# Performance work log

Measured on AMD Instinct MI355X. Metric: run time of the kernel, lower is better.

The kernel has to match this reference:

```python
import jax, jax.numpy as jnp
import numpy as np

B, N, C, H = 1, 4096, 512, 8
S = 64  # sqrt(N), static


def setup_inputs() -> dict:
    key = jax.random.key(0)
    ks = jax.random.split(key, 4)
    d = C // H
    return {
        "x": jax.random.normal(ks[0], (B, N, C), dtype=jnp.float32),
        "num_heads": H,
        "bias": jnp.zeros((1,), dtype=jnp.float32),  # unused in original forward
        "scale": jnp.asarray(d ** -0.5, dtype=jnp.float32),
        "Wqkv": jax.random.normal(ks[1], (3 * C, C), dtype=jnp.float32) * (C ** -0.5),
        "bqkv": jnp.zeros((3 * C,), dtype=jnp.float32),
        "Wproj": jax.random.normal(ks[2], (C, C), dtype=jnp.float32) * (C ** -0.5),
        "bproj": jnp.zeros((C,), dtype=jnp.float32),
    }


def reference(x, num_heads, bias, scale, Wqkv, bqkv, Wproj, bproj):
    b, n, c = x.shape
    d = c // num_heads
    # fused QKV projection: [b, n, 3c] -> [3, b, h, n, d]
    qkv = (x @ Wqkv.T + bqkv).reshape(b, n, 3, num_heads, d).transpose(2, 0, 3, 1, 4)
    q, k, v = qkv[0] * scale, qkv[1], qkv[2]
    attn = jax.nn.softmax(jnp.einsum("bhnd,bhmd->bhnm", q, k), axis=-1)
    out = jnp.einsum("bhnm,bhmd->bhnd", attn, v)
    out = out.transpose(0, 2, 1, 3).reshape(b, n, c)
    out = out @ Wproj.T + bproj
    return out.reshape(b, S, S, c)
```

## Files before the change

### kernel.cpp

```cpp
#include <hip/hip_runtime.h>
#include <stdint.h>

#define NTOK 4096
#define CDIM 512
#define HEADS 8
#define DHEAD 64
#define PHEAD (NTOK * DHEAD)

typedef __bf16 bf16x8 __attribute__((ext_vector_type(8)));
typedef float f32x4 __attribute__((ext_vector_type(4)));

__device__ __forceinline__ unsigned short bfbits(float f) {
    return __builtin_bit_cast(unsigned short, (__bf16)f);
}

__device__ __forceinline__ f32x4 mfma32(bf16x8 a, bf16x8 b, f32x4 c) {
    return __builtin_amdgcn_mfma_f32_16x16x32_bf16(a, b, c, 0, 0, 0);
}

__device__ __forceinline__ void stage8(unsigned short* dst, const float* src) {
    const float4 v0 = *(const float4*)src;
    const float4 v1 = *(const float4*)(src + 4);
    ushort4 o0, o1;
    o0.x = bfbits(v0.x); o0.y = bfbits(v0.y); o0.z = bfbits(v0.z); o0.w = bfbits(v0.w);
    o1.x = bfbits(v1.x); o1.y = bfbits(v1.y); o1.z = bfbits(v1.z); o1.w = bfbits(v1.w);
    *(ushort4*)dst = o0;
    *(ushort4*)(dst + 4) = o1;
}

__global__ __launch_bounds__(256) void gemm_qkv(
    const float* __restrict__ A,
    const float* __restrict__ Bm,
    const float* __restrict__ bias,
    const float* __restrict__ scale_p,
    unsigned short* __restrict__ qkv_out)
{
    __shared__ __align__(16) unsigned short smem[64 * 136];
    unsigned short* lA = smem;
    unsigned short* lB = smem + 2048;

    const int tid = threadIdx.x;
    const int mBase = blockIdx.y * 64, nBase = blockIdx.x * 128;
    const int lane = tid & 63;
    const int w = __builtin_amdgcn_readfirstlane(tid >> 6);
    const int l16 = lane & 15, quad = lane >> 4;
    const int srow = tid >> 2, scol = (tid & 3) * 8;

    f32x4 acc[4][2] = {};

    for (int kt = 0; kt < CDIM; kt += 32) {
        __syncthreads();
        stage8(&lA[srow * 32 + scol], &A[(size_t)(mBase + srow) * CDIM + kt + scol]);
#pragma unroll
        for (int p = 0; p < 2; ++p) {
            const int r = p * 64 + srow;
            stage8(&lB[r * 32 + scol], &Bm[(size_t)(nBase + r) * CDIM + kt + scol]);
        }
        __syncthreads();

        bf16x8 af[4], bfr[2];
#pragma unroll
        for (int i = 0; i < 4; ++i)
            af[i] = *(const bf16x8*)&lA[(i * 16 + l16) * 32 + quad * 8];
#pragma unroll
        for (int j = 0; j < 2; ++j)
            bfr[j] = *(const bf16x8*)&lB[(w * 32 + j * 16 + l16) * 32 + quad * 8];
#pragma unroll
        for (int i = 0; i < 4; ++i)
#pragma unroll
            for (int j = 0; j < 2; ++j)
                acc[i][j] = mfma32(af[i], bfr[j], acc[i][j]);
    }

    const int three = nBase >> 9;
    const float scl = scale_p[0] * 1.44269504f;
    const float mul = (three == 0) ? scl : 1.0f;

    __syncthreads();
#pragma unroll
    for (int i = 0; i < 4; ++i)
#pragma unroll
        for (int j = 0; j < 2; ++j)
#pragma unroll
            for (int r = 0; r < 4; ++r) {
                const int rl = i * 16 + quad * 4 + r;
                const int cl = w * 32 + j * 16 + l16;
                const float v = (acc[i][j][r] + bias[nBase + cl]) * mul;
                smem[rl * 136 + cl] = bfbits(v);
            }
    __syncthreads();

    const size_t base3 = (size_t)three * (PHEAD * HEADS);
    if (three < 2) {
#pragma unroll
        for (int pass = 0; pass < 4; ++pass) {
            const int idx = pass * 256 + tid;
            const int rl16 = idx & 15, qc = (idx >> 4) & 7;
            const int hsel = (idx >> 7) & 1, t16l = (idx >> 8) & 3;
            const uint4 d = *(const uint4*)&smem[(t16l * 16 + rl16) * 136 + hsel * 64 + qc * 8];
            const int hh = ((nBase >> 6) + hsel) & 7;
            const int t16 = (mBase >> 4) + t16l;
            const size_t dst = base3 + (size_t)hh * PHEAD +
                (size_t)(((t16 * 2 + (qc >> 2)) * 64 + (qc & 3) * 16 + rl16) * 8);
            *(uint4*)&qkv_out[dst] = d;
        }
    } else {
#pragma unroll
        for (int pass = 0; pass < 4; ++pass) {
            const int idx = pass * 256 + tid;
            const int l16t = idx & 15, quadt = (idx >> 4) & 3;
            const int dt = (idx >> 6) & 3, k32l = (idx >> 8) & 1, hsel = (idx >> 9) & 1;
            const int col = hsel * 64 + dt * 16 + l16t;
            unsigned short o8[8];
#pragma unroll
            for (int e = 0; e < 4; ++e) {
                o8[e]     = smem[(k32l * 32 + quadt * 4 + e) * 136 + col];
                o8[e + 4] = smem[(k32l * 32 + 16 + quadt * 4 + e) * 136 + col];
            }
            const int hh = ((nBase >> 6) + hsel) & 7;
            const int k32 = (mBase >> 5) + k32l;
            const size_t dst = base3 + (size_t)hh * PHEAD +
                (size_t)(((k32 * 4 + dt) * 64 + quadt * 16 + l16t) * 8);
            *(uint4*)&qkv_out[dst] = *(uint4*)o8;
        }
    }
}

__global__ __launch_bounds__(256, 4) void flash6_k(
    const unsigned short* __restrict__ qf,
    const unsigned short* __restrict__ kf,
    const unsigned short* __restrict__ vf,
    unsigned short* __restrict__ attn_out)
{
    __shared__ float ldsO[4][32][68];
    __shared__ float sml[4][32];

    const int tid = threadIdx.x;
    const int lane = tid & 63;
    const int w = __builtin_amdgcn_readfirstlane(tid >> 6);
    const int l16 = lane & 15, quad = lane >> 4;
    const int h = blockIdx.x, qb = blockIdx.y;

    const unsigned short* qh = qf + (size_t)h * PHEAD;
    const unsigned short* kb = kf + (size_t)h * PHEAD + w * 65536;
    const unsigned short* vb = vf + (size_t)h * PHEAD + w * 65536;

    bf16x8 qfr[2][2];
#pragma unroll
    for (int qt = 0; qt < 2; ++qt)
#pragma unroll
        for (int d2 = 0; d2 < 2; ++d2)
            qfr[qt][d2] = *(const bf16x8*)&qh[((qb * 2 + qt) * 2 + d2) * 512 + lane * 8];

    bf16x8 ones;
#pragma unroll
    for (int j = 0; j < 8; ++j) ones[j] = (__bf16)1.0f;

    f32x4 oacc[4][2] = {};
    f32x4 lacc[2] = {};

    bf16x8 kA[4], kB[4];
#pragma unroll
    for (int i = 0; i < 4; ++i)
        kA[i] = *(const bf16x8*)&kb[i * 512 + lane * 8];

    auto body = [&](int g, bf16x8* kuse, bf16x8* kload) {
#pragma unroll
        for (int i = 0; i < 4; ++i)
            kload[i] = *(const bf16x8*)&kb[(g + 1) * 2048 + i * 512 + lane * 8];
        bf16x8 vc[4];
#pragma unroll
        for (int i = 0; i < 4; ++i)
            vc[i] = *(const bf16x8*)&vb[g * 2048 + i * 512 + lane * 8];

        f32x4 s[2][2];
#pragma unroll
        for (int kt = 0; kt < 2; ++kt)
#pragma unroll
            for (int qt = 0; qt < 2; ++qt) {
                f32x4 a = {};
                a = mfma32(kuse[kt * 2 + 0], qfr[qt][0], a);
                a = mfma32(kuse[kt * 2 + 1], qfr[qt][1], a);
                s[kt][qt] = a;
            }

        bf16x8 pf[2];
#pragma unroll
        for (int qt = 0; qt < 2; ++qt) {
            bf16x8 pb;
#pragma unroll
            for (int kt = 0; kt < 2; ++kt)
#pragma unroll
                for (int r = 0; r < 4; ++r)
                    pb[kt * 4 + r] = (__bf16)__builtin_amdgcn_exp2f(s[kt][qt][r]);
            pf[qt] = pb;
            lacc[qt] = mfma32(ones, pb, lacc[qt]);
        }
#pragma unroll
        for (int dt = 0; dt < 4; ++dt)
#pragma unroll
            for (int qt = 0; qt < 2; ++qt)
                oacc[dt][qt] = mfma32(vc[dt], pf[qt], oacc[dt][qt]);
    };

    for (int it = 0; it < 16; ++it) {
        body(it * 2 + 0, kA, kB);
        body(it * 2 + 1, kB, kA);
    }

    if (quad == 0) {
#pragma unroll
        for (int qt = 0; qt < 2; ++qt) sml[w][qt * 16 + l16] = lacc[qt][0];
    }
    __syncthreads();
#pragma unroll
    for (int qt = 0; qt < 2; ++qt) {
        const int q = qt * 16 + l16;
#pragma unroll
        for (int dt = 0; dt < 4; ++dt)
            *(f32x4*)&ldsO[w][q][dt * 16 + quad * 4] = oacc[dt][qt];
    }
    __syncthreads();
    {
        const int q = tid >> 3, dseg = (tid & 7) * 8;
        const float L = sml[0][q] + sml[1][q] + sml[2][q] + sml[3][q];
        const float inv = 1.f / L;
        unsigned short o8[8];
#pragma unroll
        for (int i = 0; i < 8; ++i) {
            const float v = ldsO[0][q][dseg + i] + ldsO[1][q][dseg + i] +
                            ldsO[2][q][dseg + i] + ldsO[3][q][dseg + i];
            o8[i] = bfbits(v * inv);
        }
        *(uint4*)&attn_out[(size_t)(qb * 32 + q) * CDIM + h * DHEAD + dseg] = *(uint4*)o8;
    }
}

__global__ __launch_bounds__(256) void gemm_proj(
    const unsigned short* __restrict__ A,
    const float* __restrict__ Bm,
    const float* __restrict__ bias,
    float* __restrict__ c_out)
{
    __shared__ __align__(16) unsigned short smem[2 * 64 * 32];
    unsigned short* lA = smem;
    unsigned short* lB = smem + 2048;

    const int tid = threadIdx.x;
    const int mBase = blockIdx.y * 64, nBase = blockIdx.x * 64;
    const int lane = tid & 63;
    const int w = __builtin_amdgcn_readfirstlane(tid >> 6);
    const int l16 = lane & 15, quad = lane >> 4;
    const int srow = tid >> 2, scol = (tid & 3) * 8;

    f32x4 acc[4] = {};

    for (int kt = 0; kt < CDIM; kt += 32) {
        __syncthreads();
        *(uint4*)&lA[srow * 32 + scol] =
            *(const uint4*)&A[(size_t)(mBase + srow) * CDIM + kt + scol];
        stage8(&lB[srow * 32 + scol], &Bm[(size_t)(nBase + srow) * CDIM + kt + scol]);
        __syncthreads();

        bf16x8 af[4], bfr;
#pragma unroll
        for (int i = 0; i < 4; ++i)
            af[i] = *(const bf16x8*)&lA[(i * 16 + l16) * 32 + quad * 8];
        bfr = *(const bf16x8*)&lB[(w * 16 + l16) * 32 + quad * 8];
#pragma unroll
        for (int i = 0; i < 4; ++i)
            acc[i] = mfma32(af[i], bfr, acc[i]);
    }

#pragma unroll
    for (int i = 0; i < 4; ++i)
#pragma unroll
        for (int r = 0; r < 4; ++r) {
            const int grow = mBase + i * 16 + quad * 4 + r;
            const int gcol = nBase + w * 16 + l16;
            c_out[(size_t)grow * CDIM + gcol] = acc[i][r] + bias[gcol];
        }
}

extern "C" void kernel_launch(void* const* d_in, const int* in_sizes, int n_in,
                              void* d_out, int out_size, void* d_ws, size_t ws_size,
                              hipStream_t stream) {
    const float* x       = (const float*)d_in[0];
    const float* scale_p = (const float*)d_in[3];
    const float* Wqkv    = (const float*)d_in[4];
    const float* bqkv    = (const float*)d_in[5];
    const float* Wproj   = (const float*)d_in[6];
    const float* bproj   = (const float*)d_in[7];
    float* out = (float*)d_out;

    char* ws = (char*)d_ws;
    const size_t OFF_QKV  = 0;
    const size_t OFF_ATTN = 12582912;
    const size_t NEEDED   = OFF_ATTN + 4194304;
    if (ws_size < NEEDED) return;

    unsigned short* qkvb  = (unsigned short*)(ws + OFF_QKV);
    unsigned short* attnb = (unsigned short*)(ws + OFF_ATTN);

    gemm_qkv<<<dim3(12, 64), 256, 0, stream>>>(x, Wqkv, bqkv, scale_p, qkvb);

    const unsigned short* qfr = qkvb;
    const unsigned short* kfr = qkvb + (size_t)PHEAD * HEADS;
    const unsigned short* vfr = qkvb + (size_t)2 * PHEAD * HEADS;
    flash6_k<<<dim3(8, 128), 256, 0, stream>>>(qfr, kfr, vfr, attnb);

    gemm_proj<<<dim3(8, 64), 256, 0, stream>>>(attnb, Wproj, bproj, out);
}
```

Measured before the change: 142.8 us.

## Double query tile in flash kernel, prefetch GEMM tiles into registers, pad LDS

The attention kernel now handles 64 queries per block instead of 32, so each K/V fragment loaded from global memory feeds twice as many MFMAs. Grid size halves and occupancy bounds drop from 4 to 2 blocks per SM. Both GEMMs now prefetch the next K-slice of global data into registers while the current slice is computed. Their LDS rows are padded from 32 to 40 elements to reduce bank conflicts. The cost is higher register and LDS use, which may reduce occupancy.

```diff
diff --git a/kernel.cpp b/kernel.cpp
--- a/kernel.cpp
+++ b/kernel.cpp
@@ -6,6 +6,7 @@
 #define HEADS 8
 #define DHEAD 64
 #define PHEAD (NTOK * DHEAD)
+#define LDS_K 40
 
 typedef __bf16 bf16x8 __attribute__((ext_vector_type(8)));
 typedef float f32x4 __attribute__((ext_vector_type(4)));
@@ -18,9 +19,7 @@
     return __builtin_amdgcn_mfma_f32_16x16x32_bf16(a, b, c, 0, 0, 0);
 }
 
-__device__ __forceinline__ void stage8(unsigned short* dst, const float* src) {
-    const float4 v0 = *(const float4*)src;
-    const float4 v1 = *(const float4*)(src + 4);
+__device__ __forceinline__ void cvt_store8(unsigned short* dst, float4 v0, float4 v1) {
     ushort4 o0, o1;
     o0.x = bfbits(v0.x); o0.y = bfbits(v0.y); o0.z = bfbits(v0.z); o0.w = bfbits(v0.w);
     o1.x = bfbits(v1.x); o1.y = bfbits(v1.y); o1.z = bfbits(v1.z); o1.w = bfbits(v1.w);
@@ -37,7 +36,7 @@
 {
     __shared__ __align__(16) unsigned short smem[64 * 136];
     unsigned short* lA = smem;
-    unsigned short* lB = smem + 2048;
+    unsigned short* lB = smem + 64 * LDS_K;
 
     const int tid = threadIdx.x;
     const int mBase = blockIdx.y * 64, nBase = blockIdx.x * 128;
@@ -46,25 +45,38 @@
     const int l16 = lane & 15, quad = lane >> 4;
     const int srow = tid >> 2, scol = (tid & 3) * 8;
 
+    const float* pA  = &A[(size_t)(mBase + srow) * CDIM + scol];
+    const float* pB0 = &Bm[(size_t)(nBase + srow) * CDIM + scol];
+    const float* pB1 = &Bm[(size_t)(nBase + 64 + srow) * CDIM + scol];
+
     f32x4 acc[4][2] = {};
+
+    float4 ra0, ra1, rb00, rb01, rb10, rb11;
+    auto issue = [&](int kt) {
+        ra0  = *(const float4*)(pA + kt);
+        ra1  = *(const float4*)(pA + kt + 4);
+        rb00 = *(const float4*)(pB0 + kt);
+        rb01 = *(const float4*)(pB0 + kt + 4);
+        rb10 = *(const float4*)(pB1 + kt);
+        rb11 = *(const float4*)(pB1 + kt + 4);
+    };
+    issue(0);
 
     for (int kt = 0; kt < CDIM; kt += 32) {
         __syncthreads();
-        stage8(&lA[srow * 32 + scol], &A[(size_t)(mBase + srow) * CDIM + kt + scol]);
-#pragma unroll
-        for (int p = 0; p < 2; ++p) {
-            const int r = p * 64 + srow;
-            stage8(&lB[r * 32 + scol], &Bm[(size_t)(nBase + r) * CDIM + kt + scol]);
-        }
+        cvt_store8(&lA[srow * LDS_K + scol], ra0, ra1);
+        cvt_store8(&lB[srow * LDS_K + scol], rb00, rb01);
+        cvt_store8(&lB[(64 + srow) * LDS_K + scol], rb10, rb11);
         __syncthreads();
+        if (kt + 32 < CDIM) issue(kt + 32);
 
         bf16x8 af[4], bfr[2];
 #pragma unroll
         for (int i = 0; i < 4; ++i)
-            af[i] = *(const bf16x8*)&lA[(i * 16 + l16) * 32 + quad * 8];
+            af[i] = *(const bf16x8*)&lA[(i * 16 + l16) * LDS_K + quad * 8];
 #pragma unroll
         for (int j = 0; j < 2; ++j)
-            bfr[j] = *(const bf16x8*)&lB[(w * 32 + j * 16 + l16) * 32 + quad * 8];
+            bfr[j] = *(const bf16x8*)&lB[(w * 32 + j * 16 + l16) * LDS_K + quad * 8];
 #pragma unroll
         for (int i = 0; i < 4; ++i)
 #pragma unroll
@@ -126,14 +138,14 @@
     }
 }
 
-__global__ __launch_bounds__(256, 4) void flash6_k(
+__global__ __launch_bounds__(256, 2) void flash7_k(
     const unsigned short* __restrict__ qf,
     const unsigned short* __restrict__ kf,
     const unsigned short* __restrict__ vf,
     unsigned short* __restrict__ attn_out)
 {
-    __shared__ float ldsO[4][32][68];
-    __shared__ float sml[4][32];
+    __shared__ float ldsO[4][64][68];
+    __shared__ float sml[4][64];
 
     const int tid = threadIdx.x;
     const int lane = tid & 63;
@@ -145,19 +157,19 @@
     const unsigned short* kb = kf + (size_t)h * PHEAD + w * 65536;
     const unsigned short* vb = vf + (size_t)h * PHEAD + w * 65536;
 
-    bf16x8 qfr[2][2];
-#pragma unroll
-    for (int qt = 0; qt < 2; ++qt)
+    bf16x8 qfr[4][2];
+#pragma unroll
+    for (int qt = 0; qt < 4; ++qt)
 #pragma unroll
         for (int d2 = 0; d2 < 2; ++d2)
-            qfr[qt][d2] = *(const bf16x8*)&qh[((qb * 2 + qt) * 2 + d2) * 512 + lane * 8];
+            qfr[qt][d2] = *(const bf16x8*)&qh[((qb * 4 + qt) * 2 + d2) * 512 + lane * 8];
 
     bf16x8 ones;
 #pragma unroll
     for (int j = 0; j < 8; ++j) ones[j] = (__bf16)1.0f;
 
-    f32x4 oacc[4][2] = {};
-    f32x4 lacc[2] = {};
+    f32x4 oacc[4][4] = {};
+    f32x4 lacc[4] = {};
 
     bf16x8 kA[4], kB[4];
 #pragma unroll
@@ -173,33 +185,27 @@
         for (int i = 0; i < 4; ++i)
             vc[i] = *(const bf16x8*)&vb[g * 2048 + i * 512 + lane * 8];
 
-        f32x4 s[2][2];
-#pragma unroll
-        for (int kt = 0; kt < 2; ++kt)
-#pragma unroll
-            for (int qt = 0; qt < 2; ++qt) {
-                f32x4 a = {};
-                a = mfma32(kuse[kt * 2 + 0], qfr[qt][0], a);
-                a = mfma32(kuse[kt * 2 + 1], qfr[qt][1], a);
-                s[kt][qt] = a;
+        bf16x8 pf[4];
+#pragma unroll
+        for (int qt = 0; qt < 4; ++qt) {
+            f32x4 s0 = {}, s1 = {};
+            s0 = mfma32(kuse[0], qfr[qt][0], s0);
+            s0 = mfma32(kuse[1], qfr[qt][1], s0);
+            s1 = mfma32(kuse[2], qfr[qt][0], s1);
+            s1 = mfma32(kuse[3], qfr[qt][1], s1);
+            bf16x8 pb;
+#pragma unroll
+            for (int r = 0; r < 4; ++r) {
+                pb[r]     = (__bf16)__builtin_amdgcn_exp2f(s0[r]);
+                pb[4 + r] = (__bf16)__builtin_amdgcn_exp2f(s1[r]);
             }
-
-        bf16x8 pf[2];
-#pragma unroll
-        for (int qt = 0; qt < 2; ++qt) {
-            bf16x8 pb;
-#pragma unroll
-            for (int kt = 0; kt < 2; ++kt)
-#pragma unroll
-                for (int r = 0; r < 4; ++r)
-                    pb[kt * 4 + r] = (__bf16)__builtin_amdgcn_exp2f(s[kt][qt][r]);
             pf[qt] = pb;
             lacc[qt] = mfma32(ones, pb, lacc[qt]);
         }
 #pragma unroll
         for (int dt = 0; dt < 4; ++dt)
 #pragma unroll
-            for (int qt = 0; qt < 2; ++qt)
+            for (int qt = 0; qt < 4; ++qt)
                 oacc[dt][qt] = mfma32(vc[dt], pf[qt], oacc[dt][qt]);
     };
 
@@ -210,19 +216,20 @@
 
     if (quad == 0) {
 #pragma unroll
-        for (int qt = 0; qt < 2; ++qt) sml[w][qt * 16 + l16] = lacc[qt][0];
-    }
-    __syncthreads();
-#pragma unroll
-    for (int qt = 0; qt < 2; ++qt) {
+        for (int qt = 0; qt < 4; ++qt) sml[w][qt * 16 + l16] = lacc[qt][0];
+    }
+#pragma unroll
+    for (int qt = 0; qt < 4; ++qt) {
         const int q = qt * 16 + l16;
 #pragma unroll
         for (int dt = 0; dt < 4; ++dt)
             *(f32x4*)&ldsO[w][q][dt * 16 + quad * 4] = oacc[dt][qt];
     }
     __syncthreads();
-    {
-        const int q = tid >> 3, dseg = (tid & 7) * 8;
+#pragma unroll
+    for (int pass = 0; pass < 2; ++pass) {
+        const int idx = pass * 256 + tid;
+        const int q = idx >> 3, dseg = (idx & 7) * 8;
         const float L = sml[0][q] + sml[1][q] + sml[2][q] + sml[3][q];
         const float inv = 1.f / L;
         unsigned short o8[8];
@@ -232,7 +239,7 @@
                             ldsO[2][q][dseg + i] + ldsO[3][q][dseg + i];
             o8[i] = bfbits(v * inv);
         }
-        *(uint4*)&attn_out[(size_t)(qb * 32 + q) * CDIM + h * DHEAD + dseg] = *(uint4*)o8;
+        *(uint4*)&attn_out[(size_t)(qb * 64 + q) * CDIM + h * DHEAD + dseg] = *(uint4*)o8;
     }
 }
 
@@ -242,9 +249,9 @@
     const float* __restrict__ bias,
     float* __restrict__ c_out)
 {
-    __shared__ __align__(16) unsigned short smem[2 * 64 * 32];
+    __shared__ __align__(16) unsigned short smem[2 * 64 * LDS_K];
     unsigned short* lA = smem;
-    unsigned short* lB = smem + 2048;
+    unsigned short* lB = smem + 64 * LDS_K;
 
     const int tid = threadIdx.x;
     const int mBase = blockIdx.y * 64, nBase = blockIdx.x * 64;
@@ -253,20 +260,31 @@
     const int l16 = lane & 15, quad = lane >> 4;
     const int srow = tid >> 2, scol = (tid & 3) * 8;
 
+    const unsigned short* pA = &A[(size_t)(mBase + srow) * CDIM + scol];
+    const float* pB = &Bm[(size_t)(nBase + srow) * CDIM + scol];
+
     f32x4 acc[4] = {};
+
+    uint4 rA; float4 rb0, rb1;
+    auto issue = [&](int kt) {
+        rA  = *(const uint4*)(pA + kt);
+        rb0 = *(const float4*)(pB + kt);
+        rb1 = *(const float4*)(pB + kt + 4);
+    };
+    issue(0);
 
     for (int kt = 0; kt < CDIM; kt += 32) {
         __syncthreads();
-        *(uint4*)&lA[srow * 32 + scol] =
-            *(const uint4*)&A[(size_t)(mBase + srow) * CDIM + kt + scol];
-        stage8(&lB[srow * 32 + scol], &Bm[(size_t)(nBase + srow) * CDIM + kt + scol]);
+        *(uint4*)&lA[srow * LDS_K + scol] = rA;
+        cvt_store8(&lB[srow * LDS_K + scol], rb0, rb1);
         __syncthreads();
+        if (kt + 32 < CDIM) issue(kt + 32);
 
         bf16x8 af[4], bfr;
 #pragma unroll
         for (int i = 0; i < 4; ++i)
-            af[i] = *(const bf16x8*)&lA[(i * 16 + l16) * 32 + quad * 8];
-        bfr = *(const bf16x8*)&lB[(w * 16 + l16) * 32 + quad * 8];
+            af[i] = *(const bf16x8*)&lA[(i * 16 + l16) * LDS_K + quad * 8];
+        bfr = *(const bf16x8*)&lB[(w * 16 + l16) * LDS_K + quad * 8];
 #pragma unroll
         for (int i = 0; i < 4; ++i)
             acc[i] = mfma32(af[i], bfr, acc[i]);
@@ -307,7 +325,7 @@
     const unsigned short* qfr = qkvb;
     const unsigned short* kfr = qkvb + (size_t)PHEAD * HEADS;
     const unsigned short* vfr = qkvb + (size_t)2 * PHEAD * HEADS;
-    flash6_k<<<dim3(8, 128), 256, 0, stream>>>(qfr, kfr, vfr, attnb);
+    flash7_k<<<dim3(8, 64), 256, 0, stream>>>(qfr, kfr, vfr, attnb);
 
     gemm_proj<<<dim3(8, 64), 256, 0, stream>>>(attnb, Wproj, bproj, out);
 }
```

Result: faster. 136.1 us (-4.7%).
